# Kernel optimization log

Hardware: AMD Instinct MI355X
Metric: run time of the kernel (lower is better)

Reference implementation:

```python
import jax, jax.numpy as jnp
import numpy as np

B_, C_, H_, W_ = 4, 256, 64, 64
D_MODEL = C_ // 4        # 64, mamba d_model
D_INNER = 2 * D_MODEL    # 128, expand=2
D_STATE = 16
D_CONV = 4
DT_RANK = 4              # ceil(d_model/16)


def setup_inputs() -> dict:
    key = jax.random.key(0)
    ks = jax.random.split(key, 10)
    s = 0.02
    p = {}
    p["x"] = jax.random.normal(ks[0], (B_, C_, H_, W_), jnp.float32)
    p["norm_g"] = jnp.ones((C_,), jnp.float32)
    p["norm_b"] = jnp.zeros((C_,), jnp.float32)
    p["skip_scale"] = jnp.ones((1,), jnp.float32)
    p["proj_w"] = jax.random.normal(ks[1], (C_, C_), jnp.float32) * s
    p["proj_b"] = jnp.zeros((C_,), jnp.float32)
    p["in_proj_w"] = jax.random.normal(ks[2], (2 * D_INNER, D_MODEL), jnp.float32) * s
    p["conv_w"] = jax.random.normal(ks[3], (D_INNER, 1, D_CONV), jnp.float32) * s
    p["conv_b"] = jnp.zeros((D_INNER,), jnp.float32)
    p["x_proj_w"] = jax.random.normal(ks[4], (DT_RANK + 2 * D_STATE, D_INNER), jnp.float32) * s
    p["dt_w"] = jax.random.normal(ks[5], (D_INNER, DT_RANK), jnp.float32) * s
    p["dt_b"] = jax.random.normal(ks[6], (D_INNER,), jnp.float32) * 0.1
    # S4D-real init: A_n = n for n in 1..d_state
    p["A_log"] = jnp.log(jnp.broadcast_to(jnp.arange(1, D_STATE + 1, dtype=jnp.float32), (D_INNER, D_STATE)))
    p["D"] = jnp.ones((D_INNER,), jnp.float32)
    p["out_w"] = jax.random.normal(ks[7], (D_MODEL, D_INNER), jnp.float32) * s
    return p


def _layernorm(x, g, b, eps=1e-5):
    mu = jnp.mean(x, axis=-1, keepdims=True)
    var = jnp.mean(jnp.square(x - mu), axis=-1, keepdims=True)
    return (x - mu) * jax.lax.rsqrt(var + eps) * g + b


def _mamba(x, in_proj_w, conv_w, conv_b, x_proj_w, dt_w, dt_b, A_log, D, out_w):
    # x: [N, L, d_model]
    N, L, _ = x.shape
    xz = x @ in_proj_w.T                      # [N, L, 2*d_inner]
    xi, z = jnp.split(xz, 2, axis=-1)
    # causal depthwise conv1d over time
    xc = jax.lax.conv_general_dilated(
        xi.transpose(0, 2, 1), conv_w, (1,), [(D_CONV - 1, 0)],
        feature_group_count=D_INNER)          # [N, d_inner, L]
    u = jax.nn.silu((xc + conv_b[None, :, None]).transpose(0, 2, 1))  # [N, L, d_inner]
    dbl = u @ x_proj_w.T                      # [N, L, dt_rank + 2*d_state]
    dt, Bm, Cm = jnp.split(dbl, [DT_RANK, DT_RANK + D_STATE], axis=-1)
    delta = jax.nn.softplus(dt @ dt_w.T + dt_b)  # [N, L, d_inner]
    A = -jnp.exp(A_log)                       # [d_inner, d_state]

    def step(h, inp):
        d_t, B_t, C_t, u_t = inp              # [N,d], [N,n], [N,n], [N,d]
        dA = jnp.exp(d_t[:, :, None] * A)     # [N, d, n]
        h = dA * h + (d_t * u_t)[:, :, None] * B_t[:, None, :]
        y = jnp.einsum('bdn,bn->bd', h, C_t)
        return h, y

    h0 = jnp.zeros((N, D_INNER, D_STATE), x.dtype)
    xs = (delta.transpose(1, 0, 2), Bm.transpose(1, 0, 2),
          Cm.transpose(1, 0, 2), u.transpose(1, 0, 2))
    _, ys = jax.lax.scan(step, h0, xs)        # ys: [L, N, d_inner]
    y = ys.transpose(1, 0, 2) + u * D
    y = y * jax.nn.silu(z)
    return y @ out_w.T                        # [N, L, d_model]


def reference(x, norm_g, norm_b, skip_scale, proj_w, proj_b, in_proj_w, conv_w,
              conv_b, x_proj_w, dt_w, dt_b, A_log, D, out_w):
    B, C = x.shape[:2]
    img_dims = x.shape[2:]
    xf = x.reshape(B, C, -1).transpose(0, 2, 1)       # [B, L, C]
    xn = _layernorm(xf, norm_g, norm_b)
    parts = jnp.split(xn, 8, axis=2)
    b1 = jnp.concatenate([parts[7], parts[0]], axis=2)
    b2 = jnp.concatenate([parts[1], parts[2]], axis=2)
    b3 = jnp.concatenate([parts[3], parts[4]], axis=2)
    b4 = jnp.concatenate([parts[5], parts[6]], axis=2)
    # if_shifted_round=True: all four branches share the same mamba -> batch them
    stacked = jnp.concatenate([b1, b2, b3, b4], axis=0)  # [4B, L, C/4]
    ym = _mamba(stacked, in_proj_w, conv_w, conv_b, x_proj_w,
                dt_w, dt_b, A_log, D, out_w) + skip_scale * stacked
    m1, m2, m3, m4 = jnp.split(ym, 4, axis=0)
    t8, t1 = jnp.split(m1, 2, axis=2)
    xm = jnp.concatenate([t1, m2, m3, m4, t8], axis=2)   # [B, L, C]
    xm = _layernorm(xm, norm_g, norm_b)
    xm = xm @ proj_w.T + proj_b
    return xm.transpose(0, 2, 1).reshape(B, -1, *img_dims)
```

## Files before the change

kernel.cpp:

```cpp
#include <hip/hip_runtime.h>
#include <hip/hip_bf16.h>

#define L_ 4096
#define CCH 256
#define CH 64
#define NC 64

__global__ __launch_bounds__(256) void k1_ln_scatter(
    const float* __restrict__ x, const float* __restrict__ g,
    const float* __restrict__ bb, float* __restrict__ stacked) {
  int b = blockIdx.y;
  int l0 = blockIdx.x * 64;
  int t = threadIdx.x;
  int lane = t & 63, w = t >> 6;
  __shared__ float xs[256][65];
  __shared__ float ps[4][64], ps2[4][64];
  __shared__ float mean_s[64], rstd_s[64];
  for (int i = 0; i < 64; ++i) {
    int c = w + 4 * i;
    xs[c][lane] = x[((size_t)b * 256 + c) * L_ + l0 + lane];
  }
  __syncthreads();
  float sum = 0.f, sq = 0.f;
  for (int c = w * 64; c < w * 64 + 64; ++c) {
    float v = xs[c][lane];
    sum += v; sq += v * v;
  }
  ps[w][lane] = sum; ps2[w][lane] = sq;
  __syncthreads();
  if (w == 0) {
    float s = ps[0][lane] + ps[1][lane] + ps[2][lane] + ps[3][lane];
    float q = ps2[0][lane] + ps2[1][lane] + ps2[2][lane] + ps2[3][lane];
    float mean = s * (1.f / 256.f);
    mean_s[lane] = mean;
    rstd_s[lane] = rsqrtf(q * (1.f / 256.f) - mean * mean + 1e-5f);
  }
  __syncthreads();
  int br = w, j = lane;
  int c = (br * 64 + j + 224) & 255;
  float gv = g[c], bv = bb[c];
  float* dst = stacked + ((size_t)(br * 4 + b) * L_ + l0) * 64 + j;
  for (int l = 0; l < 64; ++l) {
    float v = (xs[c][l] - mean_s[l]) * rstd_s[l] * gv + bv;
    dst[(size_t)l * 64] = v;
  }
}

__global__ __launch_bounds__(256) void k2_inproj(
    const float* __restrict__ stacked, const float* __restrict__ w,
    float* __restrict__ xi, float* __restrict__ z) {
  int n = blockIdx.z, l0 = blockIdx.x * 64, k0 = blockIdx.y * 64;
  __shared__ float As[64][68];
  __shared__ float Ws[64][68];
  int t = threadIdx.y * 16 + threadIdx.x;
  for (int e = t; e < 4096; e += 256) {
    int r = e >> 6, c = e & 63;
    As[r][c] = stacked[((size_t)n * L_ + l0 + r) * 64 + c];
    Ws[r][c] = w[(k0 + r) * 64 + c];
  }
  __syncthreads();
  float acc[4][4] = {};
  for (int jj = 0; jj < 16; ++jj) {
    float4 a[4], bm[4];
#pragma unroll
    for (int i = 0; i < 4; i++) a[i] = *reinterpret_cast<const float4*>(&As[threadIdx.y * 4 + i][jj * 4]);
#pragma unroll
    for (int i = 0; i < 4; i++) bm[i] = *reinterpret_cast<const float4*>(&Ws[threadIdx.x * 4 + i][jj * 4]);
#pragma unroll
    for (int i = 0; i < 4; i++)
#pragma unroll
      for (int kk = 0; kk < 4; kk++)
        acc[i][kk] += a[i].x * bm[kk].x + a[i].y * bm[kk].y + a[i].z * bm[kk].z + a[i].w * bm[kk].w;
  }
  int kb = k0 + threadIdx.x * 4;
  float* dst = (kb < 128) ? xi : z;
  int kd = (kb < 128) ? kb : kb - 128;
#pragma unroll
  for (int i = 0; i < 4; i++) {
    int l = l0 + threadIdx.y * 4 + i;
    float4 v = make_float4(acc[i][0], acc[i][1], acc[i][2], acc[i][3]);
    *reinterpret_cast<float4*>(&dst[((size_t)n * L_ + l) * 128 + kd]) = v;
  }
}

__global__ __launch_bounds__(64) void k3_conv_xproj(
    const float* __restrict__ xi, const float* __restrict__ cw,
    const float* __restrict__ cb, const float* __restrict__ xw,
    const float* __restrict__ dtw, const float* __restrict__ dtb,
    float* __restrict__ u, float* __restrict__ delta,
    float* __restrict__ Bc, float* __restrict__ Cc) {
  int n = blockIdx.y, l0 = blockIdx.x * 64, t = threadIdx.x;
  __shared__ float xt[67][129];
  __shared__ float dtl[64][4];
  for (int e4 = t; e4 < 67 * 32; e4 += 64) {
    int r = e4 >> 5, c = (e4 & 31) * 4;
    int gl = l0 - 3 + r;
    float4 v = make_float4(0.f, 0.f, 0.f, 0.f);
    if (gl >= 0) v = *reinterpret_cast<const float4*>(&xi[((size_t)n * L_ + gl) * 128 + c]);
    *reinterpret_cast<float4*>(&xt[r][c]) = v;
  }
  __syncthreads();
  int l = t;
  size_t rowbase = ((size_t)n * L_ + l0 + l) * 128;
  float acc36[36] = {};
  for (int d = 0; d < 128; ++d) {
    float c0 = cw[d * 4 + 0], c1 = cw[d * 4 + 1], c2 = cw[d * 4 + 2], c3 = cw[d * 4 + 3];
    float s = cb[d] + xt[l][d] * c0 + xt[l + 1][d] * c1 + xt[l + 2][d] * c2 + xt[l + 3][d] * c3;
    float uv = s / (1.f + __expf(-s));
    u[rowbase + d] = uv;
#pragma unroll
    for (int r = 0; r < 36; ++r) acc36[r] += uv * xw[r * 128 + d];
  }
  {
    size_t base = ((size_t)n * L_ + l0 + l) * 16;
    float4* bp = reinterpret_cast<float4*>(Bc + base);
    bp[0] = make_float4(acc36[4], acc36[5], acc36[6], acc36[7]);
    bp[1] = make_float4(acc36[8], acc36[9], acc36[10], acc36[11]);
    bp[2] = make_float4(acc36[12], acc36[13], acc36[14], acc36[15]);
    bp[3] = make_float4(acc36[16], acc36[17], acc36[18], acc36[19]);
    float4* cp = reinterpret_cast<float4*>(Cc + base);
    cp[0] = make_float4(acc36[20], acc36[21], acc36[22], acc36[23]);
    cp[1] = make_float4(acc36[24], acc36[25], acc36[26], acc36[27]);
    cp[2] = make_float4(acc36[28], acc36[29], acc36[30], acc36[31]);
    cp[3] = make_float4(acc36[32], acc36[33], acc36[34], acc36[35]);
  }
  dtl[l][0] = acc36[0]; dtl[l][1] = acc36[1]; dtl[l][2] = acc36[2]; dtl[l][3] = acc36[3];
  __syncthreads();
  float4 w0 = *reinterpret_cast<const float4*>(&dtw[t * 4]);
  float4 w1 = *reinterpret_cast<const float4*>(&dtw[(t + 64) * 4]);
  float b0 = dtb[t], b1 = dtb[t + 64];
  for (int l2 = 0; l2 < 64; ++l2) {
    float q0 = dtl[l2][0], q1 = dtl[l2][1], q2 = dtl[l2][2], q3 = dtl[l2][3];
    float dv0 = b0 + q0 * w0.x + q1 * w0.y + q2 * w0.z + q3 * w0.w;
    float dv1 = b1 + q0 * w1.x + q1 * w1.y + q2 * w1.z + q3 * w1.w;
    dv0 = (dv0 > 20.f) ? dv0 : log1pf(__expf(dv0));
    dv1 = (dv1 > 20.f) ? dv1 : log1pf(__expf(dv1));
    size_t base = ((size_t)n * L_ + l0 + l2) * 128;
    delta[base + t] = dv0;
    delta[base + t + 64] = dv1;
  }
}

__global__ __launch_bounds__(128) void k4a_chunk(
    const float* __restrict__ delta, const float* __restrict__ u,
    const float* __restrict__ Bc, const float* __restrict__ A_log,
    float* __restrict__ hend, float* __restrict__ Sdelta) {
  int c = blockIdx.x, n = blockIdx.y, d = threadIdx.x;
  __shared__ float Bs[CH * 16];
  const float* bsrc = Bc + ((size_t)n * L_ + c * CH) * 16;
  for (int e = d; e < CH * 16; e += 128) Bs[e] = bsrc[e];
  float A[16];
#pragma unroll
  for (int s = 0; s < 16; ++s) A[s] = -__expf(A_log[d * 16 + s]);
  __syncthreads();

  const float* dp = delta + ((size_t)n * L_ + c * CH) * 128 + d;
  const float* up = u + ((size_t)n * L_ + c * CH) * 128 + d;
  float h[16] = {};
  float sd = 0.f;
  float dv = dp[0], uv = up[0];
  for (int l = 0; l < CH; ++l) {
    int ln = (l + 1 < CH) ? l + 1 : l;
    float dvn = dp[(size_t)ln * 128];
    float uvn = up[(size_t)ln * 128];
    sd += dv;
    float du = dv * uv;
    float bsv[16];
    *reinterpret_cast<float4*>(&bsv[0])  = *reinterpret_cast<const float4*>(&Bs[l * 16 + 0]);
    *reinterpret_cast<float4*>(&bsv[4])  = *reinterpret_cast<const float4*>(&Bs[l * 16 + 4]);
    *reinterpret_cast<float4*>(&bsv[8])  = *reinterpret_cast<const float4*>(&Bs[l * 16 + 8]);
    *reinterpret_cast<float4*>(&bsv[12]) = *reinterpret_cast<const float4*>(&Bs[l * 16 + 12]);
#pragma unroll
    for (int s = 0; s < 16; ++s)
      h[s] = fmaf(__expf(dv * A[s]), h[s], du * bsv[s]);
    dv = dvn; uv = uvn;
  }
  float* hp = hend + (((size_t)n * NC + c) * 128 + d) * 16;
  *reinterpret_cast<float4*>(&hp[0])  = make_float4(h[0], h[1], h[2], h[3]);
  *reinterpret_cast<float4*>(&hp[4])  = make_float4(h[4], h[5], h[6], h[7]);
  *reinterpret_cast<float4*>(&hp[8])  = make_float4(h[8], h[9], h[10], h[11]);
  *reinterpret_cast<float4*>(&hp[12]) = make_float4(h[12], h[13], h[14], h[15]);
  Sdelta[((size_t)n * NC + c) * 128 + d] = sd;
}

__global__ __launch_bounds__(256) void k4b_combine(
    const float* __restrict__ Sdelta, const float* __restrict__ A_log,
    float* __restrict__ hend) {
  int n = blockIdx.x >> 3, d0 = (blockIdx.x & 7) * 16;
  int d = d0 + (threadIdx.x >> 4), s = threadIdx.x & 15;
  float A = -__expf(A_log[d * 16 + s]);
  float H = 0.f;
  size_t i0 = ((size_t)n * NC) * 128 + d;
  float sd = Sdelta[i0];
  float he = hend[i0 * 16 + s];
  for (int c = 0; c < NC; ++c) {
    int cn = (c + 1 < NC) ? c + 1 : c;
    size_t in_ = ((size_t)n * NC + cn) * 128 + d;
    float sdn = Sdelta[in_];
    float hen = hend[in_ * 16 + s];
    size_t i = ((size_t)n * NC + c) * 128 + d;
    hend[i * 16 + s] = H;
    H = fmaf(__expf(A * sd), H, he);
    sd = sdn; he = hen;
  }
}

__global__ __launch_bounds__(128) void k4c_scan(
    const float* __restrict__ delta, const float* __restrict__ u,
    const float* __restrict__ Bc, const float* __restrict__ Cc,
    const float* __restrict__ A_log, const float* __restrict__ Hstart,
    float* __restrict__ y) {
  int c = blockIdx.x, n = blockIdx.y, d = threadIdx.x;
  __shared__ float Bs[CH * 16];
  __shared__ float Cs[CH * 16];
  const float* bsrc = Bc + ((size_t)n * L_ + c * CH) * 16;
  const float* csrc = Cc + ((size_t)n * L_ + c * CH) * 16;
  for (int e = d; e < CH * 16; e += 128) { Bs[e] = bsrc[e]; Cs[e] = csrc[e]; }
  float A[16];
#pragma unroll
  for (int s = 0; s < 16; ++s) A[s] = -__expf(A_log[d * 16 + s]);
  __syncthreads();

  const float* hp = Hstart + (((size_t)n * NC + c) * 128 + d) * 16;
  float h[16];
  *reinterpret_cast<float4*>(&h[0])  = *reinterpret_cast<const float4*>(&hp[0]);
  *reinterpret_cast<float4*>(&h[4])  = *reinterpret_cast<const float4*>(&hp[4]);
  *reinterpret_cast<float4*>(&h[8])  = *reinterpret_cast<const float4*>(&hp[8]);
  *reinterpret_cast<float4*>(&h[12]) = *reinterpret_cast<const float4*>(&hp[12]);

  const float* dp = delta + ((size_t)n * L_ + c * CH) * 128 + d;
  const float* up = u + ((size_t)n * L_ + c * CH) * 128 + d;
  float* yp = y + ((size_t)n * L_ + c * CH) * 128 + d;
  float dv = dp[0], uv = up[0];
  for (int l = 0; l < CH; ++l) {
    int ln = (l + 1 < CH) ? l + 1 : l;
    float dvn = dp[(size_t)ln * 128];
    float uvn = up[(size_t)ln * 128];
    float du = dv * uv;
    float bsv[16], csv[16];
    *reinterpret_cast<float4*>(&bsv[0])  = *reinterpret_cast<const float4*>(&Bs[l * 16 + 0]);
    *reinterpret_cast<float4*>(&bsv[4])  = *reinterpret_cast<const float4*>(&Bs[l * 16 + 4]);
    *reinterpret_cast<float4*>(&bsv[8])  = *reinterpret_cast<const float4*>(&Bs[l * 16 + 8]);
    *reinterpret_cast<float4*>(&bsv[12]) = *reinterpret_cast<const float4*>(&Bs[l * 16 + 12]);
    *reinterpret_cast<float4*>(&csv[0])  = *reinterpret_cast<const float4*>(&Cs[l * 16 + 0]);
    *reinterpret_cast<float4*>(&csv[4])  = *reinterpret_cast<const float4*>(&Cs[l * 16 + 4]);
    *reinterpret_cast<float4*>(&csv[8])  = *reinterpret_cast<const float4*>(&Cs[l * 16 + 8]);
    *reinterpret_cast<float4*>(&csv[12]) = *reinterpret_cast<const float4*>(&Cs[l * 16 + 12]);
    float yv = 0.f;
#pragma unroll
    for (int s = 0; s < 16; ++s) {
      h[s] = fmaf(__expf(dv * A[s]), h[s], du * bsv[s]);
      yv = fmaf(h[s], csv[s], yv);
    }
    yp[(size_t)l * 128] = yv;
    dv = dvn; uv = uvn;
  }
}

__global__ __launch_bounds__(256) void k5_gate_outproj(
    const float* __restrict__ y, const float* __restrict__ u,
    const float* __restrict__ z, const float* __restrict__ Dv,
    const float* __restrict__ ow, const float* __restrict__ stacked,
    const float* __restrict__ skip, float* __restrict__ ym) {
  int n = blockIdx.y, l0 = blockIdx.x * 64;
  __shared__ float As[64][132];
  __shared__ float Ws[64][132];
  int t = threadIdx.y * 16 + threadIdx.x;
  for (int e = t; e < 64 * 128; e += 256) {
    int r = e >> 7, c = e & 127;
    size_t idx = ((size_t)n * L_ + l0 + r) * 128 + c;
    float zz = z[idx];
    As[r][c] = (y[idx] + u[idx] * Dv[c]) * (zz / (1.f + __expf(-zz)));
    Ws[r][c] = ow[(size_t)r * 128 + c];
  }
  __syncthreads();
  float acc[4][4] = {};
  for (int jj = 0; jj < 32; ++jj) {
    float4 a[4], bm[4];
#pragma unroll
    for (int i = 0; i < 4; i++) a[i] = *reinterpret_cast<const float4*>(&As[threadIdx.y * 4 + i][jj * 4]);
#pragma unroll
    for (int i = 0; i < 4; i++) bm[i] = *reinterpret_cast<const float4*>(&Ws[threadIdx.x * 4 + i][jj * 4]);
#pragma unroll
    for (int i = 0; i < 4; i++)
#pragma unroll
      for (int kk = 0; kk < 4; kk++)
        acc[i][kk] += a[i].x * bm[kk].x + a[i].y * bm[kk].y + a[i].z * bm[kk].z + a[i].w * bm[kk].w;
  }
  float sk = skip[0];
#pragma unroll
  for (int i = 0; i < 4; i++) {
    int l = l0 + threadIdx.y * 4 + i;
    const float4 st = *reinterpret_cast<const float4*>(&stacked[((size_t)n * L_ + l) * 64 + threadIdx.x * 4]);
    float4 v = make_float4(acc[i][0] + sk * st.x, acc[i][1] + sk * st.y,
                           acc[i][2] + sk * st.z, acc[i][3] + sk * st.w);
    *reinterpret_cast<float4*>(&ym[((size_t)n * L_ + l) * 64 + threadIdx.x * 4]) = v;
  }
}

__global__ __launch_bounds__(256) void k6a_ln2(
    const float* __restrict__ ym, const float* __restrict__ g,
    const float* __restrict__ bb, float* __restrict__ xmn) {
  int b = blockIdx.y;
  int l = blockIdx.x * 4 + (threadIdx.x >> 6);
  int j = threadIdx.x & 63;
  float v[4];
  float sum = 0.f, sq = 0.f;
#pragma unroll
  for (int br = 0; br < 4; ++br) {
    v[br] = ym[((size_t)(br * 4 + b) * L_ + l) * 64 + j];
    sum += v[br]; sq += v[br] * v[br];
  }
#pragma unroll
  for (int off = 1; off < 64; off <<= 1) {
    sum += __shfl_xor(sum, off);
    sq  += __shfl_xor(sq, off);
  }
  float mean = sum * (1.f / 256.f);
  float rstd = rsqrtf(sq * (1.f / 256.f) - mean * mean + 1e-5f);
#pragma unroll
  for (int br = 0; br < 4; ++br) {
    int c = (br * 64 + j + 224) & 255;
    xmn[((size_t)b * L_ + l) * 256 + c] = (v[br] - mean) * rstd * g[c] + bb[c];
  }
}

__global__ __launch_bounds__(256) void k6b_proj(
    const float* __restrict__ xmn, const float* __restrict__ pw,
    const float* __restrict__ pb, float* __restrict__ out) {
  int b = blockIdx.z, k0 = blockIdx.y * 64, l0 = blockIdx.x * 64;
  __shared__ float As[64][68];
  __shared__ float Ws[64][68];
  int t = threadIdx.y * 16 + threadIdx.x;
  float acc[4][4] = {};
  for (int cc = 0; cc < 4; ++cc) {
    __syncthreads();
    for (int e = t; e < 4096; e += 256) {
      int r = e >> 6, c = e & 63;
      As[r][c] = xmn[((size_t)b * L_ + l0 + r) * 256 + cc * 64 + c];
      Ws[r][c] = pw[(k0 + r) * 256 + cc * 64 + c];
    }
    __syncthreads();
    for (int jj = 0; jj < 16; ++jj) {
      float4 a[4], bm[4];
#pragma unroll
      for (int i = 0; i < 4; i++) a[i] = *reinterpret_cast<const float4*>(&As[threadIdx.y * 4 + i][jj * 4]);
#pragma unroll
      for (int i = 0; i < 4; i++) bm[i] = *reinterpret_cast<const float4*>(&Ws[threadIdx.x * 4 + i][jj * 4]);
#pragma unroll
      for (int i = 0; i < 4; i++)
#pragma unroll
        for (int kk = 0; kk < 4; kk++)
          acc[i][kk] += a[i].x * bm[kk].x + a[i].y * bm[kk].y + a[i].z * bm[kk].z + a[i].w * bm[kk].w;
    }
  }
  __syncthreads();
  float* Ct = &As[0][0];
#pragma unroll
  for (int i = 0; i < 4; i++)
#pragma unroll
    for (int kk = 0; kk < 4; kk++)
      Ct[(threadIdx.y * 4 + i) * 65 + (threadIdx.x * 4 + kk)] = acc[i][kk];
  __syncthreads();
  int lane64 = t & 63, w = t >> 6;
#pragma unroll
  for (int p = 0; p < 16; ++p) {
    int row = p * 4 + w;
    out[((size_t)b * 256 + k0 + row) * L_ + l0 + lane64] = Ct[lane64 * 65 + row] + pb[k0 + row];
  }
}

extern "C" void kernel_launch(void* const* d_in, const int* in_sizes, int n_in,
                              void* d_out, int out_size, void* d_ws, size_t ws_size,
                              hipStream_t stream) {
  const float* x        = (const float*)d_in[0];
  const float* norm_g   = (const float*)d_in[1];
  const float* norm_b   = (const float*)d_in[2];
  const float* skip     = (const float*)d_in[3];
  const float* proj_w   = (const float*)d_in[4];
  const float* proj_b   = (const float*)d_in[5];
  const float* in_proj_w= (const float*)d_in[6];
  const float* conv_w   = (const float*)d_in[7];
  const float* conv_b   = (const float*)d_in[8];
  const float* x_proj_w = (const float*)d_in[9];
  const float* dt_w     = (const float*)d_in[10];
  const float* dt_b     = (const float*)d_in[11];
  const float* A_log    = (const float*)d_in[12];
  const float* Dv       = (const float*)d_in[13];
  const float* out_w    = (const float*)d_in[14];
  float* out = (float*)d_out;
  float* ws  = (float*)d_ws;

  float* stacked = ws;
  float* xi      = ws + 4194304;
  float* z       = ws + 12582912;
  float* u       = ws + 20971520;
  float* delta   = ws + 29360128;
  float* Bc      = ws + 37748736;
  float* Cc      = ws + 38797312;
  float* ym      = delta;
  float* xmn     = delta + 4194304;

  float* hend   = out;
  float* Sdelta = out + 2097152;

  k1_ln_scatter<<<dim3(64, 4), 256, 0, stream>>>(x, norm_g, norm_b, stacked);
  k2_inproj<<<dim3(64, 4, 16), dim3(16, 16), 0, stream>>>(stacked, in_proj_w, xi, z);
  k3_conv_xproj<<<dim3(64, 16), 64, 0, stream>>>(xi, conv_w, conv_b, x_proj_w,
                                                 dt_w, dt_b, u, delta, Bc, Cc);
  k4a_chunk<<<dim3(NC, 16), 128, 0, stream>>>(delta, u, Bc, A_log, hend, Sdelta);
  k4b_combine<<<128, 256, 0, stream>>>(Sdelta, A_log, hend);
  k4c_scan<<<dim3(NC, 16), 128, 0, stream>>>(delta, u, Bc, Cc, A_log, hend, xi );
  k5_gate_outproj<<<dim3(64, 16), dim3(16, 16), 0, stream>>>(xi , u, z, Dv,
                                                             out_w, stacked, skip, ym);
  k6a_ln2<<<dim3(1024, 4), 256, 0, stream>>>(ym, norm_g, norm_b, xmn);
  k6b_proj<<<dim3(64, 4, 4), dim3(16, 16), 0, stream>>>(xmn, proj_w, proj_b, out);
}
```

Before: 434.1 us.

## Restructure conv+xproj kernel to 256 threads with coalesced channel-parallel conv

The conv/x_proj kernel moves from 64 threads per block to 256. The depthwise conv now runs one thread per channel, sliding along time with register-held history. This gives coalesced global reads and writes of u instead of per-row strided stores. The x_proj reduction is split four ways across thread groups through shared memory, and the delta and B/C outputs are written by separate coalesced passes. The aim is higher occupancy and better memory coalescing, at the cost of extra shared memory and barriers.

```diff
diff --git a/kernel.cpp b/kernel.cpp
--- a/kernel.cpp
+++ b/kernel.cpp
@@ -83,61 +83,75 @@
   }
 }
 
-__global__ __launch_bounds__(64) void k3_conv_xproj(
+__global__ __launch_bounds__(256) void k3_conv_xproj(
     const float* __restrict__ xi, const float* __restrict__ cw,
     const float* __restrict__ cb, const float* __restrict__ xw,
     const float* __restrict__ dtw, const float* __restrict__ dtb,
     float* __restrict__ u, float* __restrict__ delta,
     float* __restrict__ Bc, float* __restrict__ Cc) {
-  int n = blockIdx.y, l0 = blockIdx.x * 64, t = threadIdx.x;
-  __shared__ float xt[67][129];
-  __shared__ float dtl[64][4];
-  for (int e4 = t; e4 < 67 * 32; e4 += 64) {
-    int r = e4 >> 5, c = (e4 & 31) * 4;
-    int gl = l0 - 3 + r;
-    float4 v = make_float4(0.f, 0.f, 0.f, 0.f);
-    if (gl >= 0) v = *reinterpret_cast<const float4*>(&xi[((size_t)n * L_ + gl) * 128 + c]);
-    *reinterpret_cast<float4*>(&xt[r][c]) = v;
-  }
-  __syncthreads();
-  int l = t;
-  size_t rowbase = ((size_t)n * L_ + l0 + l) * 128;
-  float acc36[36] = {};
-  for (int d = 0; d < 128; ++d) {
-    float c0 = cw[d * 4 + 0], c1 = cw[d * 4 + 1], c2 = cw[d * 4 + 2], c3 = cw[d * 4 + 3];
-    float s = cb[d] + xt[l][d] * c0 + xt[l + 1][d] * c1 + xt[l + 2][d] * c2 + xt[l + 3][d] * c3;
-    float uv = s / (1.f + __expf(-s));
-    u[rowbase + d] = uv;
-#pragma unroll
-    for (int r = 0; r < 36; ++r) acc36[r] += uv * xw[r * 128 + d];
-  }
+  int n = blockIdx.y, l0 = blockIdx.x * 64;
+  int tid = threadIdx.x;
+  __shared__ float us[64][129];
+  __shared__ float dbls[64][37];
+
   {
-    size_t base = ((size_t)n * L_ + l0 + l) * 16;
-    float4* bp = reinterpret_cast<float4*>(Bc + base);
-    bp[0] = make_float4(acc36[4], acc36[5], acc36[6], acc36[7]);
-    bp[1] = make_float4(acc36[8], acc36[9], acc36[10], acc36[11]);
-    bp[2] = make_float4(acc36[12], acc36[13], acc36[14], acc36[15]);
-    bp[3] = make_float4(acc36[16], acc36[17], acc36[18], acc36[19]);
-    float4* cp = reinterpret_cast<float4*>(Cc + base);
-    cp[0] = make_float4(acc36[20], acc36[21], acc36[22], acc36[23]);
-    cp[1] = make_float4(acc36[24], acc36[25], acc36[26], acc36[27]);
-    cp[2] = make_float4(acc36[28], acc36[29], acc36[30], acc36[31]);
-    cp[3] = make_float4(acc36[32], acc36[33], acc36[34], acc36[35]);
-  }
-  dtl[l][0] = acc36[0]; dtl[l][1] = acc36[1]; dtl[l][2] = acc36[2]; dtl[l][3] = acc36[3];
-  __syncthreads();
-  float4 w0 = *reinterpret_cast<const float4*>(&dtw[t * 4]);
-  float4 w1 = *reinterpret_cast<const float4*>(&dtw[(t + 64) * 4]);
-  float b0 = dtb[t], b1 = dtb[t + 64];
-  for (int l2 = 0; l2 < 64; ++l2) {
-    float q0 = dtl[l2][0], q1 = dtl[l2][1], q2 = dtl[l2][2], q3 = dtl[l2][3];
-    float dv0 = b0 + q0 * w0.x + q1 * w0.y + q2 * w0.z + q3 * w0.w;
-    float dv1 = b1 + q0 * w1.x + q1 * w1.y + q2 * w1.z + q3 * w1.w;
-    dv0 = (dv0 > 20.f) ? dv0 : log1pf(__expf(dv0));
-    dv1 = (dv1 > 20.f) ? dv1 : log1pf(__expf(dv1));
-    size_t base = ((size_t)n * L_ + l0 + l2) * 128;
-    delta[base + t] = dv0;
-    delta[base + t + 64] = dv1;
+    int d = tid & 127, lh = tid >> 7;
+    int ls = l0 + lh * 32;
+    const float* xp = xi + ((size_t)n * L_ + ls) * 128 + d;
+    const float4 cwv = *reinterpret_cast<const float4*>(&cw[d * 4]);
+    float cbv = cb[d];
+    float xm3 = (ls >= 3) ? xp[-3 * 128] : 0.f;
+    float xm2 = (ls >= 2) ? xp[-2 * 128] : 0.f;
+    float xm1 = (ls >= 1) ? xp[-1 * 128] : 0.f;
+    float* up = u + ((size_t)n * L_ + ls) * 128 + d;
+#pragma unroll 4
+    for (int l = 0; l < 32; ++l) {
+      float xv = xp[(size_t)l * 128];
+      float s = cbv + cwv.x * xm3 + cwv.y * xm2 + cwv.z * xm1 + cwv.w * xv;
+      float uv = s / (1.f + __expf(-s));
+      us[lh * 32 + l][d] = uv;
+      up[(size_t)l * 128] = uv;
+      xm3 = xm2; xm2 = xm1; xm1 = xv;
+    }
+  }
+  __syncthreads();
+
+  {
+    int l = tid & 63, q = tid >> 6;
+    float acc[9] = {};
+    for (int d = 0; d < 128; ++d) {
+      float uv = us[l][d];
+#pragma unroll
+      for (int r = 0; r < 9; ++r) acc[r] += uv * xw[(q * 9 + r) * 128 + d];
+    }
+#pragma unroll
+    for (int r = 0; r < 9; ++r) dbls[l][q * 9 + r] = acc[r];
+  }
+  __syncthreads();
+
+  {
+    int d = tid & 127, lh = tid >> 7;
+    const float4 wv = *reinterpret_cast<const float4*>(&dtw[d * 4]);
+    float bv = dtb[d];
+    float* dp = delta + ((size_t)n * L_ + l0 + lh * 32) * 128 + d;
+    for (int l = 0; l < 32; ++l) {
+      int lr = lh * 32 + l;
+      float q0 = dbls[lr][0], q1 = dbls[lr][1], q2 = dbls[lr][2], q3 = dbls[lr][3];
+      float dv = bv + q0 * wv.x + q1 * wv.y + q2 * wv.z + q3 * wv.w;
+      dv = (dv > 20.f) ? dv : log1pf(__expf(dv));
+      dp[(size_t)l * 128] = dv;
+    }
+  }
+
+  {
+    int s = tid & 15;
+    int which = (tid >> 4) & 1;
+    int lg = tid >> 5;
+    float* dst = which ? Cc : Bc;
+    int roff = 4 + which * 16 + s;
+    for (int l3 = lg; l3 < 64; l3 += 8) {
+      dst[((size_t)n * L_ + l0 + l3) * 16 + s] = dbls[l3][roff];
+    }
   }
 }
 
@@ -406,8 +420,8 @@
 
   k1_ln_scatter<<<dim3(64, 4), 256, 0, stream>>>(x, norm_g, norm_b, stacked);
   k2_inproj<<<dim3(64, 4, 16), dim3(16, 16), 0, stream>>>(stacked, in_proj_w, xi, z);
-  k3_conv_xproj<<<dim3(64, 16), 64, 0, stream>>>(xi, conv_w, conv_b, x_proj_w,
-                                                 dt_w, dt_b, u, delta, Bc, Cc);
+  k3_conv_xproj<<<dim3(64, 16), 256, 0, stream>>>(xi, conv_w, conv_b, x_proj_w,
+                                                  dt_w, dt_b, u, delta, Bc, Cc);
   k4a_chunk<<<dim3(NC, 16), 128, 0, stream>>>(delta, u, Bc, A_log, hend, Sdelta);
   k4b_combine<<<128, 256, 0, stream>>>(Sdelta, A_log, hend);
   k4c_scan<<<dim3(NC, 16), 128, 0, stream>>>(delta, u, Bc, Cc, A_log, hend, xi );
```

Result: faster. 403.5 us (-7.0%).
